# Optimization experiments

Hardware: AMD Instinct MI355X
Metric: run time of the kernel (lower is better)

Reference implementation:

```python
import jax, jax.numpy as jnp
import numpy as np

BUCKET_SIZE = 64  # must divide seq_len


def setup_inputs() -> dict:
    key = jax.random.key(0)
    k1, k2, k3, k4 = jax.random.split(key, 4)
    B, S, D = 4, 4096, 1024
    query = jax.random.normal(k1, (B, S, D), dtype=jnp.float32)
    key_t = jax.random.normal(k2, (B, S, D), dtype=jnp.float32)
    value = jax.random.normal(k3, (B, S, D), dtype=jnp.float32)
    # random hashing hyperplanes: [B, D, bucket_size // 2]
    R = jax.random.normal(k4, (B, D, BUCKET_SIZE // 2), dtype=jnp.float32)
    return {"query": query, "key": key_t, "value": value, "R": R}


def reference(query, key, value, R):
    B, S, D = query.shape
    # random projection: [B, S, bucket_size // 2]
    xR = jnp.einsum("bsd,bdr->bsr", query, R)
    # mirror trick -> [B, S, bucket_size]
    concat_xR = jnp.concatenate([xR, -xR], axis=-1)
    buckets = jnp.argmax(concat_xR, axis=-1)          # [B, S] int
    sticker = jnp.argsort(buckets, axis=-1)            # token permutation into buckets
    undo_sort = jnp.argsort(sticker, axis=-1)          # computed in original (unused)
    # batched gather (tf.gather batch_dims=1, axis=1)
    sorted_query = jnp.take_along_axis(query, sticker[..., None], axis=1)
    sorted_value = jnp.take_along_axis(value, sticker[..., None], axis=1)
    # tf.split(x, bucket_size, 1) then stack(axis=1) == reshape to chunks
    chunked_query = sorted_query.reshape(B, BUCKET_SIZE, S // BUCKET_SIZE, D)
    chunked_value = sorted_value.reshape(B, BUCKET_SIZE, S // BUCKET_SIZE, D)
    del undo_sort, chunked_query, chunked_value  # dead code in original; module returns sticker
    return sticker
```

## Files before the change

kernel.cpp:

```cpp
#include <hip/hip_runtime.h>


#define B_DIM 4
#define S_LEN 4096
#define D_DIM 1024
#define NRR 32
#define NBK 64
#define TMK 32
#define NC32 (S_LEN / TMK)
#define NT 8

typedef const __attribute__((address_space(1))) void* gas_t;
typedef __attribute__((address_space(3))) void* las_t;

__global__ __launch_bounds__(512, 4)
void k1_buckets(const float* __restrict__ Q, const float* __restrict__ R,
                int* __restrict__ buckets, int* __restrict__ hist)
{
    __shared__ float4 smem4[4096];
    __shared__ float xs[TMK * 33];
    __shared__ int cnt[NBK];

    const int t = threadIdx.x;
    const int b = blockIdx.x >> 7;
    const int c32 = blockIdx.x & 127;

    const int w = t >> 6;
    const int lane = t & 63;
    const int tok_t = lane >> 4;
    const int r_t = (lane >> 2) & 3;
    const int kl = lane & 3;
    const int kq = w * 4 + kl;
    const int qx = kq ^ ((tok_t & 1) << 2);

    const float4* Qg4 = (const float4*)(Q + ((size_t)b * S_LEN + c32 * TMK) * D_DIM);
    const float4* Rg4 = (const float4*)(R + (size_t)b * D_DIM * NRR);

    const float4* qsrc[2];
    const float4* rsrc[2];
#pragma unroll
    for (int i = 0; i < 2; ++i) {
        const int f = i * 512 + t;
        const int tok = f >> 5, s = f & 31;
        const int swz = (tok & 7) ^ (((tok >> 3) & 1) << 2);
        qsrc[i] = Qg4 + (size_t)tok * 256 + (s ^ swz);
        const int kloc = f >> 3, rq = f & 7;
        rsrc[i] = Rg4 + (size_t)kloc * 8 + (rq ^ ((kloc >> 2) & 3));
    }
    const int dwb = t & ~63;

#define ISSUE(TILE, D)                                                        \
    {                                                                         \
        _Pragma("unroll")                                                     \
        for (int i = 0; i < 2; ++i) {                                         \
            __builtin_amdgcn_global_load_lds(                                 \
                (gas_t)(qsrc[i] + (TILE) * 32),                               \
                (las_t)&smem4[(D) * 1024 + i * 512 + dwb], 16, 0, 0);         \
            __builtin_amdgcn_global_load_lds(                                 \
                (gas_t)(rsrc[i] + (size_t)(TILE) * 1024),                     \
                (las_t)&smem4[2048 + (D) * 1024 + i * 512 + dwb], 16, 0, 0);  \
        }                                                                     \
    }

#define COMPUTE(D)                                                            \
    {                                                                         \
        const float4* qb = smem4 + (D) * 1024;                                \
        const float4* rb = smem4 + 2048 + (D) * 1024;                         \
        float4 rv[4][2];                                                      \
        _Pragma("unroll")                                                     \
        for (int kk = 0; kk < 4; ++kk)                                        \
            _Pragma("unroll")                                                 \
            for (int p = 0; p < 2; ++p)                                       \
                rv[kk][p] = rb[kq * 32 + kk * 8 + ((r_t * 2 + p) ^ kl)];      \
        _Pragma("unroll")                                                     \
        for (int j = 0; j < 8; ++j) {                                         \
            const float4 qv = qb[tok_t * 256 + j * 32 + (qx ^ j)];            \
            _Pragma("unroll")                                                 \
            for (int kk = 0; kk < 4; ++kk) {                                  \
                const float s = kk == 0 ? qv.x : kk == 1 ? qv.y               \
                              : kk == 2 ? qv.z : qv.w;                        \
                _Pragma("unroll")                                             \
                for (int p = 0; p < 2; ++p) {                                 \
                    acc[j][p].x = fmaf(s, rv[kk][p].x, acc[j][p].x);          \
                    acc[j][p].y = fmaf(s, rv[kk][p].y, acc[j][p].y);          \
                    acc[j][p].z = fmaf(s, rv[kk][p].z, acc[j][p].z);          \
                    acc[j][p].w = fmaf(s, rv[kk][p].w, acc[j][p].w);          \
                }                                                             \
            }                                                                 \
        }                                                                     \
    }

    float4 acc[8][2];
#pragma unroll
    for (int j = 0; j < 8; ++j) {
        acc[j][0] = make_float4(0.f, 0.f, 0.f, 0.f);
        acc[j][1] = make_float4(0.f, 0.f, 0.f, 0.f);
    }

    ISSUE(0, 0)
    for (int tau = 0; tau < NT; ++tau) {
        if (tau + 1 < NT) {
            ISSUE(tau + 1, (tau + 1) & 1)
            asm volatile("s_waitcnt vmcnt(4)" ::: "memory");
        } else {
            asm volatile("s_waitcnt vmcnt(0)" ::: "memory");
        }
        __syncthreads();
        COMPUTE(tau & 1)
        __syncthreads();
    }
#undef ISSUE
#undef COMPUTE

#pragma unroll
    for (int j = 0; j < 8; ++j)
#pragma unroll
        for (int p = 0; p < 2; ++p) {
            acc[j][p].x += __shfl_xor(acc[j][p].x, 1, 64);
            acc[j][p].y += __shfl_xor(acc[j][p].y, 1, 64);
            acc[j][p].z += __shfl_xor(acc[j][p].z, 1, 64);
            acc[j][p].w += __shfl_xor(acc[j][p].w, 1, 64);
            acc[j][p].x += __shfl_xor(acc[j][p].x, 2, 64);
            acc[j][p].y += __shfl_xor(acc[j][p].y, 2, 64);
            acc[j][p].z += __shfl_xor(acc[j][p].z, 2, 64);
            acc[j][p].w += __shfl_xor(acc[j][p].w, 2, 64);
        }

    if (t < NBK) cnt[t] = 0;
    if (kl == 0) {
#pragma unroll
        for (int j = 0; j < 8; ++j) {
            const int tok = tok_t * 8 + j;
            smem4[w * 256 + tok * 8 + r_t * 2 + 0] = acc[j][0];
            smem4[w * 256 + tok * 8 + r_t * 2 + 1] = acc[j][1];
        }
    }
    __syncthreads();

    if (t < 256) {
        float4 s = smem4[t];
#pragma unroll
        for (int ww = 1; ww < 8; ++ww) {
            const float4 v = smem4[ww * 256 + t];
            s.x += v.x; s.y += v.y; s.z += v.z; s.w += v.w;
        }
        const int tok = t >> 3, r2 = t & 7;
        xs[tok * 33 + r2 * 4 + 0] = s.x;
        xs[tok * 33 + r2 * 4 + 1] = s.y;
        xs[tok * 33 + r2 * 4 + 2] = s.z;
        xs[tok * 33 + r2 * 4 + 3] = s.w;
    }
    __syncthreads();

    if (t < TMK) {
        float m1 = xs[t * 33 + 0]; int i1 = 0;
        float m2 = m1;             int i2 = 0;
#pragma unroll
        for (int r = 1; r < NRR; ++r) {
            const float v = xs[t * 33 + r];
            if (v > m1) { m1 = v; i1 = r; }
            if (v < m2) { m2 = v; i2 = r; }
        }
        const int bk = (m1 >= -m2) ? i1 : (NRR + i2);
        buckets[(size_t)b * S_LEN + c32 * TMK + t] = bk;
        atomicAdd(&cnt[bk], 1);
    }
    __syncthreads();
    if (t < NBK) hist[((size_t)b * NC32 + c32) * NBK + t] = cnt[t];
}

__global__ __launch_bounds__(256) void k2_scan(
    const int* __restrict__ hist, int* __restrict__ chunkOffset)
{
    const int t = threadIdx.x;
    const int b = t >> 6;
    const int bk = t & 63;
    const int lane = t & 63;

    int total = 0;
    for (int c = 0; c < NC32; ++c)
        total += hist[((size_t)b * NC32 + c) * NBK + bk];

    int incl = total;
#pragma unroll
    for (int off = 1; off < 64; off <<= 1) {
        int n = __shfl_up(incl, off, 64);
        if (lane >= off) incl += n;
    }
    int run = incl - total;

    for (int c = 0; c < NC32; ++c) {
        int h = hist[((size_t)b * NC32 + c) * NBK + bk];
        chunkOffset[((size_t)b * NC32 + c) * NBK + bk] = run;
        run += h;
    }
}

__global__ __launch_bounds__(256) void k3_scatter(
    const int* __restrict__ buckets, const int* __restrict__ chunkOffset,
    int* __restrict__ out)
{
    const int gid = blockIdx.x * 256 + threadIdx.x;
    const int b = gid >> 12;
    const int s = gid & (S_LEN - 1);
    const int chunk = s >> 5;
    const int lane = threadIdx.x & 63;

    const int bk = buckets[gid];

    unsigned long long m = ~0ull;
#pragma unroll
    for (int i = 0; i < 6; ++i) {
        unsigned long long bi = __ballot((bk >> i) & 1);
        m &= ((bk >> i) & 1) ? bi : ~bi;
    }
    const unsigned int m32 = (unsigned int)(m >> (lane & 32));
    const int rank = __popc(m32 & ((1u << (lane & 31)) - 1u));

    const int pos = chunkOffset[((size_t)b * NC32 + chunk) * NBK + bk] + rank;
    out[(size_t)b * S_LEN + pos] = s;
}

extern "C" void kernel_launch(void* const* d_in, const int* in_sizes, int n_in,
                              void* d_out, int out_size, void* d_ws, size_t ws_size,
                              hipStream_t stream) {
    const float* Q = (const float*)d_in[0];
    const float* R = (const float*)d_in[3];

    int* buckets     = (int*)d_ws;
    int* hist        = buckets + B_DIM * S_LEN;
    int* chunkOffset = hist + B_DIM * NC32 * NBK;

    k1_buckets<<<B_DIM * NC32, 512, 0, stream>>>(Q, R, buckets, hist);
    k2_scan   <<<1,            256, 0, stream>>>(hist, chunkOffset);
    k3_scatter<<<(B_DIM * S_LEN) / 256, 256, 0, stream>>>(buckets, chunkOffset, (int*)d_out);
}
```

Measured before the change: 42.72 us.

## Halve token tile to 16 per block, doubling grid and reworking thread mapping

Shrinks the per-block token chunk from 32 to 16 and moves k1 from 512 to 256 threads, giving 1024 blocks instead of 512 so the GPU's compute units are better filled. Each thread now covers 8 k-lanes, with a 3-step shuffle reduction. The Q LDS swizzle is dropped and the R swizzle changed. The two per-iteration __syncthreads are replaced with explicit waitcnt+s_barrier sequences. The cost is that every block re-reads the full R tile for half as many tokens, and k2 must scan a histogram twice as long.

```diff
diff --git a/kernel.cpp b/kernel.cpp
--- a/kernel.cpp
+++ b/kernel.cpp
@@ -6,75 +6,72 @@
 #define D_DIM 1024
 #define NRR 32
 #define NBK 64
-#define TMK 32
-#define NC32 (S_LEN / TMK)
+#define TMK 16
+#define NCH (S_LEN / TMK)
 #define NT 8
 
 typedef const __attribute__((address_space(1))) void* gas_t;
 typedef __attribute__((address_space(3))) void* las_t;
 
-__global__ __launch_bounds__(512, 4)
-void k1_buckets(const float* __restrict__ Q, const float* __restrict__ R,
-                int* __restrict__ buckets, int* __restrict__ hist)
+__global__ void __launch_bounds__(256) __attribute__((amdgpu_waves_per_eu(4, 4)))
+k1_buckets(const float* __restrict__ Q, const float* __restrict__ R,
+           int* __restrict__ buckets, int* __restrict__ hist)
 {
-    __shared__ float4 smem4[4096];
+    __shared__ float4 smem4[3072];
     __shared__ float xs[TMK * 33];
     __shared__ int cnt[NBK];
 
     const int t = threadIdx.x;
-    const int b = blockIdx.x >> 7;
-    const int c32 = blockIdx.x & 127;
+    const int b = blockIdx.x >> 8;
+    const int ch = blockIdx.x & 255;
 
     const int w = t >> 6;
     const int lane = t & 63;
-    const int tok_t = lane >> 4;
-    const int r_t = (lane >> 2) & 3;
-    const int kl = lane & 3;
-    const int kq = w * 4 + kl;
-    const int qx = kq ^ ((tok_t & 1) << 2);
-
-    const float4* Qg4 = (const float4*)(Q + ((size_t)b * S_LEN + c32 * TMK) * D_DIM);
+    const int tok_t = lane >> 5;
+    const int r_t = (lane >> 3) & 3;
+    const int kl = lane & 7;
+    const int kq = w * 8 + kl;
+    const int dwb = t & ~63;
+    const int rsw0 = (r_t * 2 + 0) ^ kl;
+    const int rsw1 = (r_t * 2 + 1) ^ kl;
+    const int qoff = tok_t * 256 + kq;
+    const int roff = kq * 32;
+
+    const float4* Qg4 = (const float4*)(Q + ((size_t)b * S_LEN + ch * TMK) * D_DIM);
     const float4* Rg4 = (const float4*)(R + (size_t)b * D_DIM * NRR);
-
-    const float4* qsrc[2];
-    const float4* rsrc[2];
-#pragma unroll
-    for (int i = 0; i < 2; ++i) {
-        const int f = i * 512 + t;
-        const int tok = f >> 5, s = f & 31;
-        const int swz = (tok & 7) ^ (((tok >> 3) & 1) << 2);
-        qsrc[i] = Qg4 + (size_t)tok * 256 + (s ^ swz);
-        const int kloc = f >> 3, rq = f & 7;
-        rsrc[i] = Rg4 + (size_t)kloc * 8 + (rq ^ ((kloc >> 2) & 3));
-    }
-    const int dwb = t & ~63;
 
 #define ISSUE(TILE, D)                                                        \
     {                                                                         \
         _Pragma("unroll")                                                     \
         for (int i = 0; i < 2; ++i) {                                         \
+            const int f = t + 256 * i;                                        \
             __builtin_amdgcn_global_load_lds(                                 \
-                (gas_t)(qsrc[i] + (TILE) * 32),                               \
-                (las_t)&smem4[(D) * 1024 + i * 512 + dwb], 16, 0, 0);         \
+                (gas_t)(Qg4 + (size_t)(f >> 5) * 256 + (TILE) * 32 + (f & 31)),\
+                (las_t)&smem4[(D) * 512 + (i << 8) + dwb], 16, 0, 0);         \
+        }                                                                     \
+        _Pragma("unroll")                                                     \
+        for (int i = 0; i < 4; ++i) {                                         \
+            const int f = t + 256 * i;                                        \
             __builtin_amdgcn_global_load_lds(                                 \
-                (gas_t)(rsrc[i] + (size_t)(TILE) * 1024),                     \
-                (las_t)&smem4[2048 + (D) * 1024 + i * 512 + dwb], 16, 0, 0);  \
+                (gas_t)(Rg4 + ((size_t)(TILE) * 128 + (f >> 3)) * 8           \
+                        + ((f & 7) ^ ((f >> 5) & 7))),                        \
+                (las_t)&smem4[1024 + (D) * 1024 + (i << 8) + dwb], 16, 0, 0); \
         }                                                                     \
     }
 
 #define COMPUTE(D)                                                            \
     {                                                                         \
-        const float4* qb = smem4 + (D) * 1024;                                \
-        const float4* rb = smem4 + 2048 + (D) * 1024;                         \
+        const float4* qb = smem4 + (D) * 512;                                 \
+        const float4* rb = smem4 + 1024 + (D) * 1024;                         \
         float4 rv[4][2];                                                      \
         _Pragma("unroll")                                                     \
-        for (int kk = 0; kk < 4; ++kk)                                        \
-            _Pragma("unroll")                                                 \
-            for (int p = 0; p < 2; ++p)                                       \
-                rv[kk][p] = rb[kq * 32 + kk * 8 + ((r_t * 2 + p) ^ kl)];      \
+        for (int kk = 0; kk < 4; ++kk) {                                      \
+            rv[kk][0] = rb[roff + kk * 8 + rsw0];                             \
+            rv[kk][1] = rb[roff + kk * 8 + rsw1];                             \
+        }                                                                     \
         _Pragma("unroll")                                                     \
         for (int j = 0; j < 8; ++j) {                                         \
-            const float4 qv = qb[tok_t * 256 + j * 32 + (qx ^ j)];            \
+            const float4 qv = qb[qoff + j * 32];                              \
             _Pragma("unroll")                                                 \
             for (int kk = 0; kk < 4; ++kk) {                                  \
                 const float s = kk == 0 ? qv.x : kk == 1 ? qv.y               \
@@ -101,13 +98,16 @@
     for (int tau = 0; tau < NT; ++tau) {
         if (tau + 1 < NT) {
             ISSUE(tau + 1, (tau + 1) & 1)
-            asm volatile("s_waitcnt vmcnt(4)" ::: "memory");
+            asm volatile("s_waitcnt vmcnt(6)\n\ts_barrier" ::: "memory");
         } else {
-            asm volatile("s_waitcnt vmcnt(0)" ::: "memory");
-        }
-        __syncthreads();
+            asm volatile("s_waitcnt vmcnt(0)\n\ts_barrier" ::: "memory");
+        }
         COMPUTE(tau & 1)
-        __syncthreads();
+        if (tau + 1 < NT) {
+            asm volatile("s_waitcnt lgkmcnt(0)\n\ts_barrier" ::: "memory");
+        } else {
+            __syncthreads();
+        }
     }
 #undef ISSUE
 #undef COMPUTE
@@ -116,14 +116,13 @@
     for (int j = 0; j < 8; ++j)
 #pragma unroll
         for (int p = 0; p < 2; ++p) {
-            acc[j][p].x += __shfl_xor(acc[j][p].x, 1, 64);
-            acc[j][p].y += __shfl_xor(acc[j][p].y, 1, 64);
-            acc[j][p].z += __shfl_xor(acc[j][p].z, 1, 64);
-            acc[j][p].w += __shfl_xor(acc[j][p].w, 1, 64);
-            acc[j][p].x += __shfl_xor(acc[j][p].x, 2, 64);
-            acc[j][p].y += __shfl_xor(acc[j][p].y, 2, 64);
-            acc[j][p].z += __shfl_xor(acc[j][p].z, 2, 64);
-            acc[j][p].w += __shfl_xor(acc[j][p].w, 2, 64);
+#pragma unroll
+            for (int off = 1; off < 8; off <<= 1) {
+                acc[j][p].x += __shfl_xor(acc[j][p].x, off, 64);
+                acc[j][p].y += __shfl_xor(acc[j][p].y, off, 64);
+                acc[j][p].z += __shfl_xor(acc[j][p].z, off, 64);
+                acc[j][p].w += __shfl_xor(acc[j][p].w, off, 64);
+            }
         }
 
     if (t < NBK) cnt[t] = 0;
@@ -131,24 +130,24 @@
 #pragma unroll
         for (int j = 0; j < 8; ++j) {
             const int tok = tok_t * 8 + j;
-            smem4[w * 256 + tok * 8 + r_t * 2 + 0] = acc[j][0];
-            smem4[w * 256 + tok * 8 + r_t * 2 + 1] = acc[j][1];
+            smem4[w * 128 + tok * 8 + r_t * 2 + 0] = acc[j][0];
+            smem4[w * 128 + tok * 8 + r_t * 2 + 1] = acc[j][1];
         }
     }
     __syncthreads();
 
-    if (t < 256) {
+    if (t < 128) {
         float4 s = smem4[t];
 #pragma unroll
-        for (int ww = 1; ww < 8; ++ww) {
-            const float4 v = smem4[ww * 256 + t];
+        for (int ww = 1; ww < 4; ++ww) {
+            const float4 v = smem4[ww * 128 + t];
             s.x += v.x; s.y += v.y; s.z += v.z; s.w += v.w;
         }
-        const int tok = t >> 3, r2 = t & 7;
-        xs[tok * 33 + r2 * 4 + 0] = s.x;
-        xs[tok * 33 + r2 * 4 + 1] = s.y;
-        xs[tok * 33 + r2 * 4 + 2] = s.z;
-        xs[tok * 33 + r2 * 4 + 3] = s.w;
+        const int tok = t >> 3, rq = t & 7;
+        xs[tok * 33 + rq * 4 + 0] = s.x;
+        xs[tok * 33 + rq * 4 + 1] = s.y;
+        xs[tok * 33 + rq * 4 + 2] = s.z;
+        xs[tok * 33 + rq * 4 + 3] = s.w;
     }
     __syncthreads();
 
@@ -162,11 +161,11 @@
             if (v < m2) { m2 = v; i2 = r; }
         }
         const int bk = (m1 >= -m2) ? i1 : (NRR + i2);
-        buckets[(size_t)b * S_LEN + c32 * TMK + t] = bk;
+        buckets[(size_t)b * S_LEN + ch * TMK + t] = bk;
         atomicAdd(&cnt[bk], 1);
     }
     __syncthreads();
-    if (t < NBK) hist[((size_t)b * NC32 + c32) * NBK + t] = cnt[t];
+    if (t < NBK) hist[((size_t)b * NCH + ch) * NBK + t] = cnt[t];
 }
 
 __global__ __launch_bounds__(256) void k2_scan(
@@ -178,8 +177,8 @@
     const int lane = t & 63;
 
     int total = 0;
-    for (int c = 0; c < NC32; ++c)
-        total += hist[((size_t)b * NC32 + c) * NBK + bk];
+    for (int c = 0; c < NCH; ++c)
+        total += hist[((size_t)b * NCH + c) * NBK + bk];
 
     int incl = total;
 #pragma unroll
@@ -189,9 +188,9 @@
     }
     int run = incl - total;
 
-    for (int c = 0; c < NC32; ++c) {
-        int h = hist[((size_t)b * NC32 + c) * NBK + bk];
-        chunkOffset[((size_t)b * NC32 + c) * NBK + bk] = run;
+    for (int c = 0; c < NCH; ++c) {
+        int h = hist[((size_t)b * NCH + c) * NBK + bk];
+        chunkOffset[((size_t)b * NCH + c) * NBK + bk] = run;
         run += h;
     }
 }
@@ -203,7 +202,7 @@
     const int gid = blockIdx.x * 256 + threadIdx.x;
     const int b = gid >> 12;
     const int s = gid & (S_LEN - 1);
-    const int chunk = s >> 5;
+    const int chunk = s >> 4;
     const int lane = threadIdx.x & 63;
 
     const int bk = buckets[gid];
@@ -214,10 +213,10 @@
         unsigned long long bi = __ballot((bk >> i) & 1);
         m &= ((bk >> i) & 1) ? bi : ~bi;
     }
-    const unsigned int m32 = (unsigned int)(m >> (lane & 32));
-    const int rank = __popc(m32 & ((1u << (lane & 31)) - 1u));
-
-    const int pos = chunkOffset[((size_t)b * NC32 + chunk) * NBK + bk] + rank;
+    const unsigned int m16 = (unsigned int)((m >> (lane & 48)) & 0xFFFFull);
+    const int rank = __popc(m16 & ((1u << (lane & 15)) - 1u));
+
+    const int pos = chunkOffset[((size_t)b * NCH + chunk) * NBK + bk] + rank;
     out[(size_t)b * S_LEN + pos] = s;
 }
 
@@ -229,9 +228,9 @@
 
     int* buckets     = (int*)d_ws;
     int* hist        = buckets + B_DIM * S_LEN;
-    int* chunkOffset = hist + B_DIM * NC32 * NBK;
-
-    k1_buckets<<<B_DIM * NC32, 512, 0, stream>>>(Q, R, buckets, hist);
-    k2_scan   <<<1,            256, 0, stream>>>(hist, chunkOffset);
+    int* chunkOffset = hist + B_DIM * NCH * NBK;
+
+    k1_buckets<<<B_DIM * NCH, 256, 0, stream>>>(Q, R, buckets, hist);
+    k2_scan   <<<1,           256, 0, stream>>>(hist, chunkOffset);
     k3_scatter<<<(B_DIM * S_LEN) / 256, 256, 0, stream>>>(buckets, chunkOffset, (int*)d_out);
 }
```

Measured after the change: 48.91 us. 14.5% more time.

## Restructure bucket projection kernel: per-wave token ownership with staged R quarters

Applied to the files above, without the earlier changes.

Rewrites the projection GEMM kernel to use 256 threads. Each wave now owns 8 tokens and splits the D dimension across 16 lanes. R is staged into LDS a quarter of D at a time and shared by all waves, while each wave streams its own Q rows through a private double buffer. This drops the cross-wave LDS reduction in favour of an in-wave shuffle reduction and reduces block-wide barriers inside the main loop. In exchange there are more shuffle steps, lower thread count per block, and a full stall each time an R quarter is reloaded.

```diff
diff --git a/kernel.cpp b/kernel.cpp
--- a/kernel.cpp
+++ b/kernel.cpp
@@ -8,17 +8,17 @@
 #define NBK 64
 #define TMK 32
 #define NC32 (S_LEN / TMK)
-#define NT 8
+#define QOFF 2048
 
 typedef const __attribute__((address_space(1))) void* gas_t;
 typedef __attribute__((address_space(3))) void* las_t;
 
-__global__ __launch_bounds__(512, 4)
-void k1_buckets(const float* __restrict__ Q, const float* __restrict__ R,
-                int* __restrict__ buckets, int* __restrict__ hist)
+__global__ void __launch_bounds__(256) __attribute__((amdgpu_waves_per_eu(2, 2)))
+k1_buckets(const float* __restrict__ Q, const float* __restrict__ R,
+           int* __restrict__ buckets, int* __restrict__ hist)
 {
-    __shared__ float4 smem4[4096];
-    __shared__ float xs[TMK * 33];
+    __shared__ float4 smem4[QOFF + 1024];
+    __shared__ float xs[TMK * 36];
     __shared__ int cnt[NBK];
 
     const int t = threadIdx.x;
@@ -27,64 +27,62 @@
 
     const int w = t >> 6;
     const int lane = t & 63;
-    const int tok_t = lane >> 4;
-    const int r_t = (lane >> 2) & 3;
-    const int kl = lane & 3;
-    const int kq = w * 4 + kl;
-    const int qx = kq ^ ((tok_t & 1) << 2);
-
-    const float4* Qg4 = (const float4*)(Q + ((size_t)b * S_LEN + c32 * TMK) * D_DIM);
+    const int r_t = lane >> 4;
+    const int kl = lane & 15;
+
+    const float4* Qw4 = (const float4*)(Q + ((size_t)b * S_LEN + c32 * TMK + w * 8) * D_DIM);
     const float4* Rg4 = (const float4*)(R + (size_t)b * D_DIM * NRR);
 
-    const float4* qsrc[2];
-    const float4* rsrc[2];
-#pragma unroll
-    for (int i = 0; i < 2; ++i) {
-        const int f = i * 512 + t;
-        const int tok = f >> 5, s = f & 31;
-        const int swz = (tok & 7) ^ (((tok >> 3) & 1) << 2);
-        qsrc[i] = Qg4 + (size_t)tok * 256 + (s ^ swz);
-        const int kloc = f >> 3, rq = f & 7;
-        rsrc[i] = Rg4 + (size_t)kloc * 8 + (rq ^ ((kloc >> 2) & 3));
-    }
-    const int dwb = t & ~63;
-
-#define ISSUE(TILE, D)                                                        \
+    const int qwoff = QOFF + w * 256;
+    const int rbase = (kl >> 1) * 64 + (kl & 1) * 32;
+    const int rx0 = (r_t * 2 + 0) ^ (kl >> 1);
+    const int rx1 = (r_t * 2 + 1) ^ (kl >> 1);
+
+#define STAGE_R(QTR)                                                          \
     {                                                                         \
         _Pragma("unroll")                                                     \
+        for (int i = 0; i < 8; ++i) {                                         \
+            __builtin_amdgcn_global_load_lds(                                 \
+                (gas_t)(Rg4 + ((size_t)(QTR) * 256 + (w * 8 + i) * 8          \
+                               + (lane >> 3)) * 8 + ((lane & 7) ^ i)),        \
+                (las_t)&smem4[w * 512 + i * 64 + lane], 16, 0, 0);            \
+        }                                                                     \
+    }
+
+#define ISSUE_Q(TAU, BUF)                                                     \
+    {                                                                         \
+        _Pragma("unroll")                                                     \
         for (int i = 0; i < 2; ++i) {                                         \
+            const int s = i * 64 + lane;                                      \
             __builtin_amdgcn_global_load_lds(                                 \
-                (gas_t)(qsrc[i] + (TILE) * 32),                               \
-                (las_t)&smem4[(D) * 1024 + i * 512 + dwb], 16, 0, 0);         \
-            __builtin_amdgcn_global_load_lds(                                 \
-                (gas_t)(rsrc[i] + (size_t)(TILE) * 1024),                     \
-                (las_t)&smem4[2048 + (D) * 1024 + i * 512 + dwb], 16, 0, 0);  \
-        }                                                                     \
-    }
-
-#define COMPUTE(D)                                                            \
+                (gas_t)(Qw4 + (size_t)(s >> 4) * 256 + (TAU) * 16 + (s & 15)),\
+                (las_t)&smem4[qwoff + (BUF) * 128 + s], 16, 0, 0);            \
+        }                                                                     \
+    }
+
+#define COMPUTE(TL, BUF)                                                      \
     {                                                                         \
-        const float4* qb = smem4 + (D) * 1024;                                \
-        const float4* rb = smem4 + 2048 + (D) * 1024;                         \
+        const float4* rb = smem4 + (TL) * 512 + rbase;                        \
+        const float4* qb = smem4 + qwoff + (BUF) * 128 + kl;                  \
         float4 rv[4][2];                                                      \
         _Pragma("unroll")                                                     \
-        for (int kk = 0; kk < 4; ++kk)                                        \
+        for (int c = 0; c < 4; ++c) {                                         \
+            rv[c][0] = rb[c * 8 + rx0];                                       \
+            rv[c][1] = rb[c * 8 + rx1];                                       \
+        }                                                                     \
+        _Pragma("unroll")                                                     \
+        for (int j = 0; j < 8; ++j) {                                         \
+            const float4 qv = qb[j * 16];                                     \
             _Pragma("unroll")                                                 \
-            for (int p = 0; p < 2; ++p)                                       \
-                rv[kk][p] = rb[kq * 32 + kk * 8 + ((r_t * 2 + p) ^ kl)];      \
-        _Pragma("unroll")                                                     \
-        for (int j = 0; j < 8; ++j) {                                         \
-            const float4 qv = qb[tok_t * 256 + j * 32 + (qx ^ j)];            \
-            _Pragma("unroll")                                                 \
-            for (int kk = 0; kk < 4; ++kk) {                                  \
-                const float s = kk == 0 ? qv.x : kk == 1 ? qv.y               \
-                              : kk == 2 ? qv.z : qv.w;                        \
+            for (int c = 0; c < 4; ++c) {                                     \
+                const float s = c == 0 ? qv.x : c == 1 ? qv.y                 \
+                              : c == 2 ? qv.z : qv.w;                         \
                 _Pragma("unroll")                                             \
                 for (int p = 0; p < 2; ++p) {                                 \
-                    acc[j][p].x = fmaf(s, rv[kk][p].x, acc[j][p].x);          \
-                    acc[j][p].y = fmaf(s, rv[kk][p].y, acc[j][p].y);          \
-                    acc[j][p].z = fmaf(s, rv[kk][p].z, acc[j][p].z);          \
-                    acc[j][p].w = fmaf(s, rv[kk][p].w, acc[j][p].w);          \
+                    acc[j][p].x = fmaf(s, rv[c][p].x, acc[j][p].x);           \
+                    acc[j][p].y = fmaf(s, rv[c][p].y, acc[j][p].y);           \
+                    acc[j][p].z = fmaf(s, rv[c][p].z, acc[j][p].z);           \
+                    acc[j][p].w = fmaf(s, rv[c][p].w, acc[j][p].w);           \
                 }                                                             \
             }                                                                 \
         }                                                                     \
@@ -96,68 +94,63 @@
         acc[j][0] = make_float4(0.f, 0.f, 0.f, 0.f);
         acc[j][1] = make_float4(0.f, 0.f, 0.f, 0.f);
     }
-
-    ISSUE(0, 0)
-    for (int tau = 0; tau < NT; ++tau) {
-        if (tau + 1 < NT) {
-            ISSUE(tau + 1, (tau + 1) & 1)
-            asm volatile("s_waitcnt vmcnt(4)" ::: "memory");
-        } else {
+    if (t < NBK) cnt[t] = 0;
+
+    STAGE_R(0)
+    ISSUE_Q(0, 0)
+    ISSUE_Q(1, 1)
+    asm volatile("s_waitcnt vmcnt(0)" ::: "memory");
+    __syncthreads();
+
+    int tau = 0;
+    for (int qtr = 0; qtr < 4; ++qtr) {
+        if (qtr) {
+            __syncthreads();
+            STAGE_R(qtr)
             asm volatile("s_waitcnt vmcnt(0)" ::: "memory");
-        }
-        __syncthreads();
-        COMPUTE(tau & 1)
-        __syncthreads();
-    }
-#undef ISSUE
+            __syncthreads();
+        }
+#pragma unroll
+        for (int tl = 0; tl < 4; ++tl, ++tau) {
+            asm volatile("s_waitcnt vmcnt(2)" ::: "memory");
+            COMPUTE(tl, tau & 1)
+            asm volatile("s_waitcnt lgkmcnt(0)" ::: "memory");
+            if (tau + 2 < 16) ISSUE_Q(tau + 2, tau & 1)
+        }
+    }
+#undef STAGE_R
+#undef ISSUE_Q
 #undef COMPUTE
 
 #pragma unroll
     for (int j = 0; j < 8; ++j)
 #pragma unroll
-        for (int p = 0; p < 2; ++p) {
-            acc[j][p].x += __shfl_xor(acc[j][p].x, 1, 64);
-            acc[j][p].y += __shfl_xor(acc[j][p].y, 1, 64);
-            acc[j][p].z += __shfl_xor(acc[j][p].z, 1, 64);
-            acc[j][p].w += __shfl_xor(acc[j][p].w, 1, 64);
-            acc[j][p].x += __shfl_xor(acc[j][p].x, 2, 64);
-            acc[j][p].y += __shfl_xor(acc[j][p].y, 2, 64);
-            acc[j][p].z += __shfl_xor(acc[j][p].z, 2, 64);
-            acc[j][p].w += __shfl_xor(acc[j][p].w, 2, 64);
-        }
-
-    if (t < NBK) cnt[t] = 0;
+        for (int p = 0; p < 2; ++p)
+#pragma unroll
+            for (int off = 1; off < 16; off <<= 1) {
+                acc[j][p].x += __shfl_xor(acc[j][p].x, off, 64);
+                acc[j][p].y += __shfl_xor(acc[j][p].y, off, 64);
+                acc[j][p].z += __shfl_xor(acc[j][p].z, off, 64);
+                acc[j][p].w += __shfl_xor(acc[j][p].w, off, 64);
+            }
+
+    __syncthreads();
     if (kl == 0) {
+        float4* xsf4 = (float4*)xs;
 #pragma unroll
         for (int j = 0; j < 8; ++j) {
-            const int tok = tok_t * 8 + j;
-            smem4[w * 256 + tok * 8 + r_t * 2 + 0] = acc[j][0];
-            smem4[w * 256 + tok * 8 + r_t * 2 + 1] = acc[j][1];
-        }
-    }
-    __syncthreads();
-
-    if (t < 256) {
-        float4 s = smem4[t];
-#pragma unroll
-        for (int ww = 1; ww < 8; ++ww) {
-            const float4 v = smem4[ww * 256 + t];
-            s.x += v.x; s.y += v.y; s.z += v.z; s.w += v.w;
-        }
-        const int tok = t >> 3, r2 = t & 7;
-        xs[tok * 33 + r2 * 4 + 0] = s.x;
-        xs[tok * 33 + r2 * 4 + 1] = s.y;
-        xs[tok * 33 + r2 * 4 + 2] = s.z;
-        xs[tok * 33 + r2 * 4 + 3] = s.w;
+            xsf4[(w * 8 + j) * 9 + r_t * 2 + 0] = acc[j][0];
+            xsf4[(w * 8 + j) * 9 + r_t * 2 + 1] = acc[j][1];
+        }
     }
     __syncthreads();
 
     if (t < TMK) {
-        float m1 = xs[t * 33 + 0]; int i1 = 0;
+        float m1 = xs[t * 36 + 0]; int i1 = 0;
         float m2 = m1;             int i2 = 0;
 #pragma unroll
         for (int r = 1; r < NRR; ++r) {
-            const float v = xs[t * 33 + r];
+            const float v = xs[t * 36 + r];
             if (v > m1) { m1 = v; i1 = r; }
             if (v < m2) { m2 = v; i2 = r; }
         }
@@ -231,7 +224,7 @@
     int* hist        = buckets + B_DIM * S_LEN;
     int* chunkOffset = hist + B_DIM * NC32 * NBK;
 
-    k1_buckets<<<B_DIM * NC32, 512, 0, stream>>>(Q, R, buckets, hist);
+    k1_buckets<<<B_DIM * NC32, 256, 0, stream>>>(Q, R, buckets, hist);
     k2_scan   <<<1,            256, 0, stream>>>(hist, chunkOffset);
     k3_scatter<<<(B_DIM * S_LEN) / 256, 256, 0, stream>>>(buckets, chunkOffset, (int*)d_out);
 }
```

After: 95.80 us. 2.24x slower.
